# Kernel optimization log

Hardware: AMD Instinct MI355X
Metric: run time of the kernel (lower is better)

Reference implementation:

```python
import jax, jax.numpy as jnp
import numpy as np


def _xavier(key, shape):
    fan_out, fan_in = shape[0], shape[1]
    lim = np.sqrt(6.0 / (fan_in + fan_out)).astype(np.float32)
    return jax.random.uniform(key, shape, jnp.float32, -lim, lim)


def setup_inputs() -> dict:
    key = jax.random.key(0)
    ks = jax.random.split(key, 28)
    B, D, G, ND = 16384, 32, 6, 8
    V_user, V_item, V_gender, V_age, V_occ, V_genre = 1000000, 100000, 2, 7, 21, 19
    H1, H2 = 128, 64
    deep_in = 6 * D + ND  # 200
    return {
        "user_id": jax.random.randint(ks[0], (B,), 0, V_user),
        "item_id": jax.random.randint(ks[1], (B,), 0, V_item),
        "user_gender": jax.random.randint(ks[2], (B,), 0, V_gender),
        "user_age": jax.random.randint(ks[3], (B,), 0, V_age),
        "user_occupation": jax.random.randint(ks[4], (B,), 0, V_occ),
        "item_genre_ids": jax.random.randint(ks[5], (B, G), 0, V_genre),
        "item_genre_mask": jax.random.randint(ks[6], (B, G), 0, 2).astype(jnp.float32),
        "dense_features": jax.random.normal(ks[7], (B, ND), jnp.float32),
        # first-order (1-dim) embedding tables
        "fo_user": _xavier(ks[8], (V_user, 1)),
        "fo_item": _xavier(ks[9], (V_item, 1)),
        "fo_gender": _xavier(ks[10], (V_gender, 1)),
        "fo_age": _xavier(ks[11], (V_age, 1)),
        "fo_occ": _xavier(ks[12], (V_occ, 1)),
        "fo_genre": _xavier(ks[13], (V_genre, 1)),
        # second-order / deep embedding tables
        "emb_user": _xavier(ks[14], (V_user, D)),
        "emb_item": _xavier(ks[15], (V_item, D)),
        "emb_gender": _xavier(ks[16], (V_gender, D)),
        "emb_age": _xavier(ks[17], (V_age, D)),
        "emb_occ": _xavier(ks[18], (V_occ, D)),
        "emb_genre": _xavier(ks[19], (V_genre, D)),
        # dense linear + deep MLP
        "dense_W": _xavier(ks[20], (1, ND)),
        "dense_b": jnp.zeros((1,), jnp.float32),
        "W1": _xavier(ks[21], (H1, deep_in)),
        "b1": jnp.zeros((H1,), jnp.float32),
        "W2": _xavier(ks[22], (H2, H1)),
        "b2": jnp.zeros((H2,), jnp.float32),
        "Wout": _xavier(ks[23], (1, H2)),
        "bout": jnp.zeros((1,), jnp.float32),
    }


def _pool(table, ids, mask):
    # masked mean-pool over the genre list axis
    e = table[ids]                       # [B, G, d]
    m = mask[..., None]                  # [B, G, 1]
    denom = jnp.clip(m.sum(axis=1), 1.0)  # [B, 1]
    return (e * m).sum(axis=1) / denom   # [B, d]


def reference(user_id, item_id, user_gender, user_age, user_occupation,
              item_genre_ids, item_genre_mask, dense_features,
              fo_user, fo_item, fo_gender, fo_age, fo_occ, fo_genre,
              emb_user, emb_item, emb_gender, emb_age, emb_occ, emb_genre,
              dense_W, dense_b, W1, b1, W2, b2, Wout, bout):
    # FM first order: sum of 1-dim gathers + pooled genre + dense linear -> [B,1]
    first = (fo_user[user_id] + fo_item[item_id] + fo_gender[user_gender]
             + fo_age[user_age] + fo_occ[user_occupation]
             + _pool(fo_genre, item_genre_ids, item_genre_mask)
             + dense_features @ dense_W.T + dense_b)
    # FM second order: stack field embeddings [B, 6, D]
    x = jnp.stack([emb_user[user_id], emb_item[item_id], emb_gender[user_gender],
                   emb_age[user_age], emb_occ[user_occupation],
                   _pool(emb_genre, item_genre_ids, item_genre_mask)], axis=1)
    s = x.sum(axis=1)                                   # [B, D]
    second = 0.5 * (s * s - (x * x).sum(axis=1)).sum(axis=1, keepdims=True)  # [B,1]
    # deep part (dropout is identity in eval mode)
    deep_in = jnp.concatenate([x.reshape(x.shape[0], -1), dense_features], axis=1)
    h = jax.nn.relu(deep_in @ W1.T + b1)
    h = jax.nn.relu(h @ W2.T + b2)
    deep = h @ Wout.T + bout                            # [B,1]
    return (first + second + deep).squeeze(1)           # [B]
```

## Files before the change

### kernel.cpp

```cpp
#include <hip/hip_runtime.h>


typedef float v2f __attribute__((ext_vector_type(2)));

#define WAVES_PER_BLOCK 4
#define ROWS_PER_WAVE 8
#define ROWS_PER_BLOCK 32

__global__ void pack_weights(const float* __restrict__ W1, const float* __restrict__ W2,
                             float4* __restrict__ W1p, float4* __restrict__ W2p) {
    const int idx = blockIdx.x * blockDim.x + threadIdx.x;
    if (idx < 6400) {
        const int w = idx / 1600, rem = idx % 1600;
        const int k4 = rem >> 5, jp = rem & 31;
        const int j = w * 32 + jp;
        const float* r = W1 + j * 200 + 4 * k4;
        W1p[idx] = make_float4(r[0], r[1], r[2], r[3]);
    }
    if (idx < 2048) {
        const int w = idx / 512, rem = idx % 512;
        const int k4 = rem >> 4, jp = rem & 15;
        const int j = w * 16 + jp;
        const float* r = W2 + j * 128 + 4 * k4;
        W2p[idx] = make_float4(r[0], r[1], r[2], r[3]);
    }
}

__global__ __launch_bounds__(256) void deepfm_kernel(
    const int* __restrict__ user_id, const int* __restrict__ item_id,
    const int* __restrict__ gender_, const int* __restrict__ age_,
    const int* __restrict__ occ_, const int* __restrict__ genre_ids,
    const float* __restrict__ genre_mask, const float* __restrict__ dense,
    const float* __restrict__ fo_user, const float* __restrict__ fo_item,
    const float* __restrict__ fo_gender, const float* __restrict__ fo_age,
    const float* __restrict__ fo_occ, const float* __restrict__ fo_genre,
    const float* __restrict__ emb_user, const float* __restrict__ emb_item,
    const float* __restrict__ emb_gender, const float* __restrict__ emb_age,
    const float* __restrict__ emb_occ, const float* __restrict__ emb_genre,
    const float* __restrict__ dense_W, const float* __restrict__ dense_b,
    const float4* __restrict__ W1p, const float* __restrict__ b1,
    const float4* __restrict__ W2p, const float* __restrict__ b2,
    const float* __restrict__ Wout, const float* __restrict__ bout,
    float* __restrict__ out, int B)
{
    __shared__ float lds_di[ROWS_PER_BLOCK][200];
    __shared__ float lds_rs[ROWS_PER_BLOCK];
    __shared__ float lds_part[ROWS_PER_BLOCK][WAVES_PER_BLOCK];

    const int tid = threadIdx.x;
    const int wid = tid >> 6;
    const int lane = tid & 63;
    const int blockRow0 = blockIdx.x * ROWS_PER_BLOCK;

    {
        const int rowBase = blockRow0 + wid * ROWS_PER_WAVE;
        int uid[ROWS_PER_WAVE], iid[ROWS_PER_WAVE], gg[ROWS_PER_WAVE],
            aa[ROWS_PER_WAVE], oo[ROWS_PER_WAVE];
        #pragma unroll
        for (int r = 0; r < ROWS_PER_WAVE; ++r) {
            int row = rowBase + r; if (row >= B) row = B - 1;
            uid[r] = user_id[row]; iid[r] = item_id[row];
            gg[r] = gender_[row];  aa[r] = age_[row];  oo[r] = occ_[row];
        }

        #pragma unroll
        for (int r = 0; r < ROWS_PER_WAVE; ++r) {
            int row = rowBase + r; if (row >= B) row = B - 1;
            const int ri = wid * ROWS_PER_WAVE + r;

            int gid[6]; float mk[6]; float msum = 0.f;
            #pragma unroll
            for (int t = 0; t < 6; ++t) {
                gid[t] = genre_ids[row * 6 + t];
                mk[t]  = genre_mask[row * 6 + t];
                msum  += mk[t];
            }
            const float inv_den = 1.0f / fmaxf(msum, 1.0f);

            float pe_sum = 0.f, pe_sq = 0.f;
            {
                float v = (lane < 32) ? emb_user[(size_t)uid[r] * 32 + lane]
                                      : emb_item[(size_t)iid[r] * 32 + (lane - 32)];
                lds_di[ri][lane] = v;
                pe_sum += v; pe_sq += v * v;
            }
            {
                float v = (lane < 32) ? emb_gender[gg[r] * 32 + lane]
                                      : emb_age[aa[r] * 32 + (lane - 32)];
                lds_di[ri][64 + lane] = v;
                pe_sum += v; pe_sq += v * v;
            }
            {
                float v;
                if (lane < 32) {
                    v = emb_occ[oo[r] * 32 + lane];
                } else {
                    const int d = lane - 32;
                    float s = 0.f;
                    #pragma unroll
                    for (int t = 0; t < 6; ++t) s += mk[t] * emb_genre[gid[t] * 32 + d];
                    v = s * inv_den;
                }
                lds_di[ri][128 + lane] = v;
                pe_sum += v; pe_sq += v * v;
            }
            if (lane < 8) lds_di[ri][192 + lane] = dense[(size_t)row * 8 + lane];

            float s2 = pe_sum + __shfl_xor(pe_sum, 32);
            float ss = pe_sq  + __shfl_xor(pe_sq, 32);
            float t2 = 0.5f * (s2 * s2 - ss);
            #pragma unroll
            for (int off = 16; off >= 1; off >>= 1) t2 += __shfl_xor(t2, off);

            float fo = fo_user[uid[r]] + fo_item[iid[r]] + fo_gender[gg[r]]
                     + fo_age[aa[r]] + fo_occ[oo[r]];
            float fg = 0.f;
            #pragma unroll
            for (int t = 0; t < 6; ++t) fg += mk[t] * fo_genre[gid[t]];
            fo += fg * inv_den;
            float dd = 0.f;
            #pragma unroll
            for (int j = 0; j < 8; ++j) dd += dense[(size_t)row * 8 + j] * dense_W[j];
            fo += dd + dense_b[0];

            if (lane == 0) lds_rs[ri] = fo + t2;
        }
    }
    __syncthreads();

    const int jp1 = lane & 31;
    const int half = lane >> 5;

    v2f acc[16];
    #pragma unroll
    for (int rp = 0; rp < 16; ++rp) acc[rp] = (v2f)(0.f);

    {
        const float4* __restrict__ W1b = W1p + wid * 1600;
        const float4* __restrict__ dv = reinterpret_cast<const float4*>(&lds_di[0][0]);

        for (int k4 = 0; k4 < 50; ++k4) {
            const float4 w = W1b[k4 * 32 + jp1];
            const v2f w01 = { w.x, w.y }, w23 = { w.z, w.w };
            #pragma unroll
            for (int rp = 0; rp < 16; ++rp) {
                const float4 a = dv[(half * 16 + rp) * 50 + k4];
                const v2f a01 = { a.x, a.y }, a23 = { a.z, a.w };
                acc[rp] = __builtin_elementwise_fma(w01, a01, acc[rp]);
                acc[rp] = __builtin_elementwise_fma(w23, a23, acc[rp]);
            }
        }
    }
    __syncthreads();

    float* __restrict__ h1b = &lds_di[0][0];
    {
        const float bb = b1[wid * 32 + jp1];
        #pragma unroll
        for (int rp = 0; rp < 16; ++rp) {
            const float h = fmaxf(acc[rp].x + acc[rp].y + bb, 0.f);
            h1b[(half * 16 + rp) * 128 + wid * 32 + jp1] = h;
        }
    }
    __syncthreads();

    const int jp2 = lane & 15;
    const int rg = lane >> 4;

    v2f acc2[8];
    #pragma unroll
    for (int ri = 0; ri < 8; ++ri) acc2[ri] = (v2f)(0.f);

    {
        const float4* __restrict__ W2b = W2p + wid * 512;
        const float4* __restrict__ h1v = reinterpret_cast<const float4*>(h1b);

        for (int k4 = 0; k4 < 32; ++k4) {
            const float4 w = W2b[k4 * 16 + jp2];
            const v2f w01 = { w.x, w.y }, w23 = { w.z, w.w };
            #pragma unroll
            for (int ri = 0; ri < 8; ++ri) {
                const float4 h = h1v[(rg * 8 + ri) * 32 + k4];
                const v2f h01 = { h.x, h.y }, h23 = { h.z, h.w };
                acc2[ri] = __builtin_elementwise_fma(w01, h01, acc2[ri]);
                acc2[ri] = __builtin_elementwise_fma(w23, h23, acc2[ri]);
            }
        }
    }

    {
        const float bb2 = b2[wid * 16 + jp2];
        const float wo  = Wout[wid * 16 + jp2];
        #pragma unroll
        for (int ri = 0; ri < 8; ++ri) {
            const float h2 = fmaxf(acc2[ri].x + acc2[ri].y + bb2, 0.f);
            float v = wo * h2;
            v += __shfl_xor(v, 1); v += __shfl_xor(v, 2);
            v += __shfl_xor(v, 4); v += __shfl_xor(v, 8);
            if (jp2 == 0) lds_part[rg * 8 + ri][wid] = v;
        }
    }
    __syncthreads();

    if (tid < ROWS_PER_BLOCK) {
        const int row = blockRow0 + tid;
        if (row < B) {
            const float deep = lds_part[tid][0] + lds_part[tid][1]
                             + lds_part[tid][2] + lds_part[tid][3] + bout[0];
            out[row] = deep + lds_rs[tid];
        }
    }
}

extern "C" void kernel_launch(void* const* d_in, const int* in_sizes, int n_in,
                              void* d_out, int out_size, void* d_ws, size_t ws_size,
                              hipStream_t stream) {
    const int B = in_sizes[0];

    float4* W1p = reinterpret_cast<float4*>(d_ws);
    float4* W2p = reinterpret_cast<float4*>((char*)d_ws + 102400);

    pack_weights<<<25, 256, 0, stream>>>(
        (const float*)d_in[22], (const float*)d_in[24], W1p, W2p);

    const int grid = (B + ROWS_PER_BLOCK - 1) / ROWS_PER_BLOCK;
    deepfm_kernel<<<grid, 256, 0, stream>>>(
        (const int*)d_in[0],  (const int*)d_in[1],  (const int*)d_in[2],
        (const int*)d_in[3],  (const int*)d_in[4],  (const int*)d_in[5],
        (const float*)d_in[6],  (const float*)d_in[7],
        (const float*)d_in[8],  (const float*)d_in[9],  (const float*)d_in[10],
        (const float*)d_in[11], (const float*)d_in[12], (const float*)d_in[13],
        (const float*)d_in[14], (const float*)d_in[15], (const float*)d_in[16],
        (const float*)d_in[17], (const float*)d_in[18], (const float*)d_in[19],
        (const float*)d_in[20], (const float*)d_in[21],
        W1p, (const float*)d_in[23],
        W2p, (const float*)d_in[25],
        (const float*)d_in[26], (const float*)d_in[27],
        (float*)d_out, B);
}
```

Measured before the change: 280.8 us.

## Remap MLP register tiles to two columns per thread and pad LDS rows

```diff
diff --git a/kernel.cpp b/kernel.cpp
--- a/kernel.cpp
+++ b/kernel.cpp
@@ -2,27 +2,27 @@
 
 
 typedef float v2f __attribute__((ext_vector_type(2)));
-
-#define WAVES_PER_BLOCK 4
+static __device__ __forceinline__ v2f bc2(float x) { v2f r; r.x = x; r.y = x; return r; }
+
+#define ROWS_PER_BLOCK 32
 #define ROWS_PER_WAVE 8
-#define ROWS_PER_BLOCK 32
+#define DI_STRIDE 204
+#define H1_STRIDE 132
 
 __global__ void pack_weights(const float* __restrict__ W1, const float* __restrict__ W2,
                              float4* __restrict__ W1p, float4* __restrict__ W2p) {
     const int idx = blockIdx.x * blockDim.x + threadIdx.x;
     if (idx < 6400) {
-        const int w = idx / 1600, rem = idx % 1600;
-        const int k4 = rem >> 5, jp = rem & 31;
-        const int j = w * 32 + jp;
-        const float* r = W1 + j * 200 + 4 * k4;
-        W1p[idx] = make_float4(r[0], r[1], r[2], r[3]);
+        const int s = idx & 1, jp = (idx >> 1) & 15, k4 = (idx >> 5) % 50, w = idx / 1600;
+        const int j0 = w * 32 + 2 * jp, c = 4 * k4 + 2 * s;
+        W1p[idx] = make_float4(W1[j0 * 200 + c],     W1[(j0 + 1) * 200 + c],
+                               W1[j0 * 200 + c + 1], W1[(j0 + 1) * 200 + c + 1]);
     }
     if (idx < 2048) {
-        const int w = idx / 512, rem = idx % 512;
-        const int k4 = rem >> 4, jp = rem & 15;
-        const int j = w * 16 + jp;
-        const float* r = W2 + j * 128 + 4 * k4;
-        W2p[idx] = make_float4(r[0], r[1], r[2], r[3]);
+        const int s = idx & 1, jp = (idx >> 1) & 7, k4 = (idx >> 4) & 31, w = idx >> 9;
+        const int j0 = w * 16 + 2 * jp, c = 4 * k4 + 2 * s;
+        W2p[idx] = make_float4(W2[j0 * 128 + c],     W2[(j0 + 1) * 128 + c],
+                               W2[j0 * 128 + c + 1], W2[(j0 + 1) * 128 + c + 1]);
     }
 }
 
@@ -43,9 +43,9 @@
     const float* __restrict__ Wout, const float* __restrict__ bout,
     float* __restrict__ out, int B)
 {
-    __shared__ float lds_di[ROWS_PER_BLOCK][200];
+    __shared__ float lds_di[ROWS_PER_BLOCK][DI_STRIDE];
     __shared__ float lds_rs[ROWS_PER_BLOCK];
-    __shared__ float lds_part[ROWS_PER_BLOCK][WAVES_PER_BLOCK];
+    __shared__ float lds_part[ROWS_PER_BLOCK][4];
 
     const int tid = threadIdx.x;
     const int wid = tid >> 6;
@@ -128,26 +128,29 @@
     }
     __syncthreads();
 
-    const int jp1 = lane & 31;
-    const int half = lane >> 5;
-
-    v2f acc[16];
+    const int jp1 = lane & 15;
+    const int rh  = lane >> 4;
+
+    v2f acc[ROWS_PER_WAVE];
     #pragma unroll
-    for (int rp = 0; rp < 16; ++rp) acc[rp] = (v2f)(0.f);
+    for (int r = 0; r < ROWS_PER_WAVE; ++r) acc[r] = bc2(0.f);
 
     {
         const float4* __restrict__ W1b = W1p + wid * 1600;
         const float4* __restrict__ dv = reinterpret_cast<const float4*>(&lds_di[0][0]);
 
         for (int k4 = 0; k4 < 50; ++k4) {
-            const float4 w = W1b[k4 * 32 + jp1];
-            const v2f w01 = { w.x, w.y }, w23 = { w.z, w.w };
-            #pragma unroll
-            for (int rp = 0; rp < 16; ++rp) {
-                const float4 a = dv[(half * 16 + rp) * 50 + k4];
-                const v2f a01 = { a.x, a.y }, a23 = { a.z, a.w };
-                acc[rp] = __builtin_elementwise_fma(w01, a01, acc[rp]);
-                acc[rp] = __builtin_elementwise_fma(w23, a23, acc[rp]);
+            const float4 wa = W1b[(k4 * 16 + jp1) * 2 + 0];
+            const float4 wb = W1b[(k4 * 16 + jp1) * 2 + 1];
+            const v2f w0 = { wa.x, wa.y }, w1 = { wa.z, wa.w };
+            const v2f w2 = { wb.x, wb.y }, w3 = { wb.z, wb.w };
+            #pragma unroll
+            for (int r = 0; r < ROWS_PER_WAVE; ++r) {
+                const float4 a = dv[(rh + 4 * r) * 51 + k4];
+                acc[r] = __builtin_elementwise_fma(w0, bc2(a.x), acc[r]);
+                acc[r] = __builtin_elementwise_fma(w1, bc2(a.y), acc[r]);
+                acc[r] = __builtin_elementwise_fma(w2, bc2(a.z), acc[r]);
+                acc[r] = __builtin_elementwise_fma(w3, bc2(a.w), acc[r]);
             }
         }
     }
@@ -155,49 +158,55 @@
 
     float* __restrict__ h1b = &lds_di[0][0];
     {
-        const float bb = b1[wid * 32 + jp1];
-        #pragma unroll
-        for (int rp = 0; rp < 16; ++rp) {
-            const float h = fmaxf(acc[rp].x + acc[rp].y + bb, 0.f);
-            h1b[(half * 16 + rp) * 128 + wid * 32 + jp1] = h;
-        }
-    }
-    __syncthreads();
-
-    const int jp2 = lane & 15;
-    const int rg = lane >> 4;
-
-    v2f acc2[8];
+        const int j0 = wid * 32 + 2 * jp1;
+        const float2 bb = *reinterpret_cast<const float2*>(b1 + j0);
+        #pragma unroll
+        for (int r = 0; r < ROWS_PER_WAVE; ++r) {
+            const int row = rh + 4 * r;
+            reinterpret_cast<float2*>(h1b)[(row * H1_STRIDE + j0) >> 1] =
+                make_float2(fmaxf(acc[r].x + bb.x, 0.f), fmaxf(acc[r].y + bb.y, 0.f));
+        }
+    }
+    __syncthreads();
+
+    const int jp2 = lane & 7;
+    const int rh2 = lane >> 3;
+
+    v2f acc2[4];
     #pragma unroll
-    for (int ri = 0; ri < 8; ++ri) acc2[ri] = (v2f)(0.f);
+    for (int t = 0; t < 4; ++t) acc2[t] = bc2(0.f);
 
     {
         const float4* __restrict__ W2b = W2p + wid * 512;
         const float4* __restrict__ h1v = reinterpret_cast<const float4*>(h1b);
 
         for (int k4 = 0; k4 < 32; ++k4) {
-            const float4 w = W2b[k4 * 16 + jp2];
-            const v2f w01 = { w.x, w.y }, w23 = { w.z, w.w };
-            #pragma unroll
-            for (int ri = 0; ri < 8; ++ri) {
-                const float4 h = h1v[(rg * 8 + ri) * 32 + k4];
-                const v2f h01 = { h.x, h.y }, h23 = { h.z, h.w };
-                acc2[ri] = __builtin_elementwise_fma(w01, h01, acc2[ri]);
-                acc2[ri] = __builtin_elementwise_fma(w23, h23, acc2[ri]);
-            }
-        }
-    }
-
-    {
-        const float bb2 = b2[wid * 16 + jp2];
-        const float wo  = Wout[wid * 16 + jp2];
-        #pragma unroll
-        for (int ri = 0; ri < 8; ++ri) {
-            const float h2 = fmaxf(acc2[ri].x + acc2[ri].y + bb2, 0.f);
-            float v = wo * h2;
-            v += __shfl_xor(v, 1); v += __shfl_xor(v, 2);
-            v += __shfl_xor(v, 4); v += __shfl_xor(v, 8);
-            if (jp2 == 0) lds_part[rg * 8 + ri][wid] = v;
+            const float4 wa = W2b[(k4 * 8 + jp2) * 2 + 0];
+            const float4 wb = W2b[(k4 * 8 + jp2) * 2 + 1];
+            const v2f w0 = { wa.x, wa.y }, w1 = { wa.z, wa.w };
+            const v2f w2 = { wb.x, wb.y }, w3 = { wb.z, wb.w };
+            #pragma unroll
+            for (int t = 0; t < 4; ++t) {
+                const float4 h = h1v[(rh2 + 8 * t) * 33 + k4];
+                acc2[t] = __builtin_elementwise_fma(w0, bc2(h.x), acc2[t]);
+                acc2[t] = __builtin_elementwise_fma(w1, bc2(h.y), acc2[t]);
+                acc2[t] = __builtin_elementwise_fma(w2, bc2(h.z), acc2[t]);
+                acc2[t] = __builtin_elementwise_fma(w3, bc2(h.w), acc2[t]);
+            }
+        }
+    }
+
+    {
+        const int j0 = wid * 16 + 2 * jp2;
+        const float2 bb2 = *reinterpret_cast<const float2*>(b2 + j0);
+        const float2 wo  = *reinterpret_cast<const float2*>(Wout + j0);
+        #pragma unroll
+        for (int t = 0; t < 4; ++t) {
+            const float h2x = fmaxf(acc2[t].x + bb2.x, 0.f);
+            const float h2y = fmaxf(acc2[t].y + bb2.y, 0.f);
+            float v = wo.x * h2x + wo.y * h2y;
+            v += __shfl_xor(v, 1); v += __shfl_xor(v, 2); v += __shfl_xor(v, 4);
+            if (jp2 == 0) lds_part[rh2 + 8 * t][wid] = v;
         }
     }
     __syncthreads();
```

Measured after the change: 262.0 us. 6.7% less time.
